# Kernel optimization log

Hardware: AMD Instinct MI355X
Metric: run time of the kernel (lower is better)

Reference implementation:

```python
import jax, jax.numpy as jnp
import numpy as np

D_MODEL = 1024
N_HEADS = 16
HEAD_DIM = D_MODEL // N_HEADS
B, T = 4, 2048
EPS = 1e-5


def _layernorm(x, w, b):
    mu = jnp.mean(x, axis=-1, keepdims=True)
    var = jnp.mean(jnp.square(x - mu), axis=-1, keepdims=True)
    return (x - mu) * jax.lax.rsqrt(var + EPS) * w + b


def _heads(x, w, b):
    # x: [B,T,D]; w stored [in,out] so y = x @ w + b (== torch Linear)
    y = x @ w + b
    return y.reshape(B, T, N_HEADS, HEAD_DIM).transpose(0, 2, 1, 3)  # [B,H,T,hd]


def _attention(q, k, v):
    scores = jnp.einsum('bhqd,bhkd->bhqk', q, k) / np.sqrt(HEAD_DIM).astype(np.float32)
    attn = jax.nn.softmax(scores, axis=-1)  # dropout is identity in eval mode
    o = jnp.einsum('bhqk,bhkd->bhqd', attn, v)
    return o.transpose(0, 2, 1, 3).reshape(B, T, D_MODEL)


def setup_inputs() -> dict:
    key = jax.random.key(0)
    ks = jax.random.split(key, 16)
    s = 1.0 / np.sqrt(D_MODEL)
    def lin(k, din, dout):
        kw, kb = jax.random.split(k)
        return (jax.random.uniform(kw, (din, dout), jnp.float32, -s, s),
                jax.random.uniform(kb, (dout,), jnp.float32, -s, s))
    inp = {}
    inp['temporal_tokens'] = jax.random.normal(ks[0], (B, T, D_MODEL), jnp.float32)
    inp['feature_tokens'] = jax.random.normal(ks[1], (B, T, D_MODEL), jnp.float32)
    names = ['qt', 'kf', 'vf', 'qf', 'kt', 'vt', 'ot', 'of']
    for i, n in enumerate(names):
        w, b = lin(ks[2 + i], D_MODEL, D_MODEL)
        inp[n + '_w'], inp[n + '_b'] = w, b
    inp['fus1_w'], inp['fus1_b'] = lin(ks[10], 2 * D_MODEL, D_MODEL)
    inp['fus2_w'], inp['fus2_b'] = lin(ks[11], D_MODEL, D_MODEL)
    for n in ['ln_fus', 'ln_t', 'ln_f']:
        inp[n + '_w'] = jnp.ones((D_MODEL,), jnp.float32)
        inp[n + '_b'] = jnp.zeros((D_MODEL,), jnp.float32)
    return inp


def reference(temporal_tokens, feature_tokens,
              qt_w, qt_b, kf_w, kf_b, vf_w, vf_b,
              qf_w, qf_b, kt_w, kt_b, vt_w, vt_b,
              ot_w, ot_b, of_w, of_b,
              fus1_w, fus1_b, fus2_w, fus2_b,
              ln_fus_w, ln_fus_b, ln_t_w, ln_t_b, ln_f_w, ln_f_b):
    # temporal -> feature cross attention
    Qt = _heads(temporal_tokens, qt_w, qt_b)
    Kf = _heads(feature_tokens, kf_w, kf_b)
    Vf = _heads(feature_tokens, vf_w, vf_b)
    attn_t = _attention(Qt, Kf, Vf) @ ot_w + ot_b
    fused_t = _layernorm(temporal_tokens + attn_t, ln_t_w, ln_t_b)
    # feature -> temporal cross attention
    Qf = _heads(feature_tokens, qf_w, qf_b)
    Kt = _heads(temporal_tokens, kt_w, kt_b)
    Vt = _heads(temporal_tokens, vt_w, vt_b)
    attn_f = _attention(Qf, Kt, Vt) @ of_w + of_b
    fused_f = _layernorm(feature_tokens + attn_f, ln_f_w, ln_f_b)
    # fusion MLP
    combined = jnp.concatenate([fused_t, fused_f], axis=-1)  # [B,T,2D]
    h = jax.nn.gelu(combined @ fus1_w + fus1_b, approximate=False)
    fused = _layernorm(h @ fus2_w + fus2_b, ln_fus_w, ln_fus_b)
    return fused
```

## Files before the change

### kernel.cpp

```cpp
#include <hip/hip_runtime.h>
#include <math.h>

typedef __attribute__((ext_vector_type(8))) short short8;
typedef __attribute__((ext_vector_type(4))) short short4v;
typedef __attribute__((ext_vector_type(4))) float floatx4;

#define GLOBAL_AS __attribute__((address_space(1)))
#define LDS_AS __attribute__((address_space(3)))

__device__ __forceinline__ float bf2f(unsigned short u) {
    unsigned int x = ((unsigned int)u) << 16;
    return __builtin_bit_cast(float, x);
}
__device__ __forceinline__ unsigned short f2bf(float f) {
    unsigned int u = __builtin_bit_cast(unsigned int, f);
    u += 0x7fffu + ((u >> 16) & 1u);
    return (unsigned short)(u >> 16);
}

__global__ __launch_bounds__(256) void cvt2_kernel(
    const float* __restrict__ a, const float* __restrict__ b,
    unsigned short* __restrict__ oa, unsigned short* __restrict__ ob)
{
    const int bx = blockIdx.x;
    const float* in = bx < 8192 ? a : b;
    unsigned short* out = bx < 8192 ? oa : ob;
    const size_t i = ((size_t)(bx & 8191) * 256 + threadIdx.x) * 4;
    float4 f = *(const float4*)(in + i);
    unsigned short o[4] = {f2bf(f.x), f2bf(f.y), f2bf(f.z), f2bf(f.w)};
    *(uint2*)(out + i) = *(const uint2*)o;
}

struct WX {
    const float* src[10];
    unsigned long long dst[10];
    int r64[10];
    int cum[11];
};

__global__ __launch_bounds__(256) void transpose_all_kernel(WX P, unsigned short* __restrict__ base)
{
    __shared__ unsigned short T[64][72];
    const int bx = blockIdx.x;
    int w = 0;
    #pragma unroll
    for (int i = 0; i < 10; ++i) if (bx >= P.cum[i + 1]) w = i + 1;
    const int tix = bx - P.cum[w];
    const int R = P.r64[w] * 64;
    const int r0 = (tix >> 4) * 64, c0 = (tix & 15) * 64;
    const float* in = P.src[w];
    unsigned short* out = base + P.dst[w];
    const int t = threadIdx.x;
    {
        const int r = t >> 2, cc = (t & 3) * 16;
        const float* p = in + (size_t)(r0 + r) * 1024 + c0 + cc;
        #pragma unroll
        for (int j = 0; j < 16; j += 4) {
            float4 f = *(const float4*)(p + j);
            T[cc + j + 0][r] = f2bf(f.x);
            T[cc + j + 1][r] = f2bf(f.y);
            T[cc + j + 2][r] = f2bf(f.z);
            T[cc + j + 3][r] = f2bf(f.w);
        }
    }
    __syncthreads();
    {
        const int c = t >> 2, rr = (t & 3) * 16;
        unsigned short* q = out + (size_t)(c0 + c) * R + r0 + rr;
        *(uint4*)(q)     = *(const uint4*)(&T[c][rr]);
        *(uint4*)(q + 8) = *(const uint4*)(&T[c][rr + 8]);
    }
}

#define GEMM_CORE(A_, B_, Kdim)                                               \
    const int tid = threadIdx.x;                                              \
    const int wave = tid >> 6, lane = tid & 63;                               \
    const int quad = lane >> 4, l16 = lane & 15;                              \
    const int wm = (wave & 1) * 64, wn = (wave >> 1) * 64;                    \
    const int srow8 = lane >> 3, c8 = lane & 7;                               \
    const int scol = (c8 ^ srow8) * 8;                                        \
    floatx4 acc[4][4];                                                        \
    _Pragma("unroll")                                                         \
    for (int i = 0; i < 4; ++i)                                               \
        _Pragma("unroll")                                                     \
        for (int j = 0; j < 4; ++j) acc[i][j] = (floatx4){0.f, 0.f, 0.f, 0.f};\
    const unsigned short* pa[4];                                              \
    const unsigned short* pb[4];                                              \
    _Pragma("unroll")                                                         \
    for (int i = 0; i < 4; ++i) {                                             \
        pa[i] = (A_) + (size_t)(bm + i * 32 + wave * 8 + srow8) * (Kdim) + scol; \
        pb[i] = (B_) + (size_t)(bn + i * 32 + wave * 8 + srow8) * (Kdim) + scol; \
    }                                                                         \
    int aoff[4][2], boff[4][2];                                               \
    _Pragma("unroll")                                                         \
    for (int i = 0; i < 4; ++i)                                               \
        _Pragma("unroll")                                                     \
        for (int s = 0; s < 2; ++s) {                                         \
            const int cg = ((s * 4 + quad) ^ (l16 & 7)) * 8;                  \
            aoff[i][s] = (wm + i * 16 + l16) * 64 + cg;                       \
            boff[i][s] = (wn + i * 16 + l16) * 64 + cg;                       \
        }                                                                     \
    for (int k0 = 0; k0 < (Kdim); k0 += 64) {                                 \
        _Pragma("unroll")                                                     \
        for (int i = 0; i < 4; ++i) {                                         \
            __builtin_amdgcn_global_load_lds((const GLOBAL_AS void*)(pa[i] + k0), \
                (LDS_AS void*)(As + i * 2048 + wave * 512), 16, 0, 0);        \
            __builtin_amdgcn_global_load_lds((const GLOBAL_AS void*)(pb[i] + k0), \
                (LDS_AS void*)(Bs + i * 2048 + wave * 512), 16, 0, 0);        \
        }                                                                     \
        __syncthreads();                                                      \
        _Pragma("unroll")                                                     \
        for (int s = 0; s < 2; ++s) {                                         \
            short8 af[4], bf[4];                                              \
            _Pragma("unroll")                                                 \
            for (int i = 0; i < 4; ++i) {                                     \
                af[i] = *(const short8*)&As[aoff[i][s]];                      \
                bf[i] = *(const short8*)&Bs[boff[i][s]];                      \
            }                                                                 \
            _Pragma("unroll")                                                 \
            for (int mi = 0; mi < 4; ++mi)                                    \
                _Pragma("unroll")                                             \
                for (int ni = 0; ni < 4; ++ni)                                \
                    acc[mi][ni] = __builtin_amdgcn_mfma_f32_16x16x32_bf16(    \
                        bf[ni], af[mi], acc[mi][ni], 0, 0, 0);                \
        }                                                                     \
        __syncthreads();                                                      \
    }

template <int MODE>
__global__ __launch_bounds__(256) void gemm_kernel(
    const unsigned short* __restrict__ A,
    const unsigned short* __restrict__ Wt,
    const float* __restrict__ bias,
    unsigned short* __restrict__ C,
    int N, int K)
{
    __shared__ unsigned short As[128 * 64];
    __shared__ unsigned short Bs[128 * 64];
    const int bm = blockIdx.x * 128, bn = blockIdx.y * 128;
    GEMM_CORE(A, Wt, K)

    float4 bv[4];
    #pragma unroll
    for (int ni = 0; ni < 4; ++ni)
        bv[ni] = *(const float4*)&bias[bn + wn + ni * 16 + quad * 4];
    #pragma unroll
    for (int mi = 0; mi < 4; ++mi) {
        const int m = bm + wm + mi * 16 + l16;
        #pragma unroll
        for (int ni = 0; ni < 4; ++ni) {
            const int n0 = bn + wn + ni * 16 + quad * 4;
            float v[4];
            #pragma unroll
            for (int r = 0; r < 4; ++r) v[r] = acc[mi][ni][r] + ((const float*)&bv[ni])[r];
            if (MODE == 2) {
                #pragma unroll
                for (int r = 0; r < 4; ++r)
                    v[r] = 0.5f * v[r] * (1.0f + erff(v[r] * 0.70710678118f));
            }
            unsigned short o[4] = {f2bf(v[0]), f2bf(v[1]), f2bf(v[2]), f2bf(v[3])};
            *(uint2*)&C[(size_t)m * N + n0] = *(const uint2*)o;
        }
    }
}

__global__ __launch_bounds__(256) void gemm_out_kernel(
    const unsigned short* __restrict__ A0, const unsigned short* __restrict__ W0,
    const float* __restrict__ bi0, const float* __restrict__ r0, unsigned short* __restrict__ C0,
    const unsigned short* __restrict__ A1, const unsigned short* __restrict__ W1,
    const float* __restrict__ bi1, const float* __restrict__ r1, unsigned short* __restrict__ C1)
{
    __shared__ unsigned short As[128 * 64];
    __shared__ unsigned short Bs[128 * 64];
    const int s1 = blockIdx.y >> 3;
    const unsigned short* A = s1 ? A1 : A0;
    const unsigned short* Wt = s1 ? W1 : W0;
    const float* bias = s1 ? bi1 : bi0;
    const float* resid = s1 ? r1 : r0;
    unsigned short* C = s1 ? C1 : C0;
    const int bm = blockIdx.x * 128, bn = (blockIdx.y & 7) * 128;
    GEMM_CORE(A, Wt, 1024)

    float4 bv[4];
    #pragma unroll
    for (int ni = 0; ni < 4; ++ni)
        bv[ni] = *(const float4*)&bias[bn + wn + ni * 16 + quad * 4];
    #pragma unroll
    for (int mi = 0; mi < 4; ++mi) {
        const int m = bm + wm + mi * 16 + l16;
        #pragma unroll
        for (int ni = 0; ni < 4; ++ni) {
            const int n0 = bn + wn + ni * 16 + quad * 4;
            float4 rv = *(const float4*)&resid[(size_t)m * 1024 + n0];
            float v[4];
            v[0] = acc[mi][ni][0] + ((const float*)&bv[ni])[0] + rv.x;
            v[1] = acc[mi][ni][1] + ((const float*)&bv[ni])[1] + rv.y;
            v[2] = acc[mi][ni][2] + ((const float*)&bv[ni])[2] + rv.z;
            v[3] = acc[mi][ni][3] + ((const float*)&bv[ni])[3] + rv.w;
            unsigned short o[4] = {f2bf(v[0]), f2bf(v[1]), f2bf(v[2]), f2bf(v[3])};
            *(uint2*)&C[(size_t)m * 1024 + n0] = *(const uint2*)o;
        }
    }
}

__global__ __launch_bounds__(256) void gemm_qkv_kernel(
    const unsigned short* __restrict__ At, const unsigned short* __restrict__ Wt3t,
    const float* __restrict__ tb0, const float* __restrict__ tb1, const float* __restrict__ tb2,
    unsigned short* __restrict__ to0, unsigned short* __restrict__ to1, unsigned short* __restrict__ to2,
    const unsigned short* __restrict__ Af, const unsigned short* __restrict__ Wt3f,
    const float* __restrict__ fb0, const float* __restrict__ fb1, const float* __restrict__ fb2,
    unsigned short* __restrict__ fo0, unsigned short* __restrict__ fo1, unsigned short* __restrict__ fo2,
    float scale0)
{
    __shared__ unsigned short As[128 * 64];
    __shared__ unsigned short Bs[128 * 64];
    const int str = blockIdx.y >= 24;
    const unsigned short* A = str ? Af : At;
    const unsigned short* Wt = str ? Wt3f : Wt3t;
    const int byy = str ? (blockIdx.y - 24) : blockIdx.y;
    const int buf = byy >> 3;
    const int bn = byy * 128;
    const int cn = (byy & 7) * 128;
    const float* bias = str ? (buf == 0 ? fb0 : (buf == 1 ? fb1 : fb2))
                            : (buf == 0 ? tb0 : (buf == 1 ? tb1 : tb2));
    unsigned short* C = str ? (buf == 0 ? fo0 : (buf == 1 ? fo1 : fo2))
                            : (buf == 0 ? to0 : (buf == 1 ? to1 : to2));
    const float scale = buf == 0 ? scale0 : 1.0f;
    const int bm = blockIdx.x * 128;
    GEMM_CORE(A, Wt, 1024)

    float4 bv[4];
    #pragma unroll
    for (int ni = 0; ni < 4; ++ni)
        bv[ni] = *(const float4*)&bias[cn + wn + ni * 16 + quad * 4];
    #pragma unroll
    for (int mi = 0; mi < 4; ++mi) {
        const int m = bm + wm + mi * 16 + l16;
        #pragma unroll
        for (int ni = 0; ni < 4; ++ni) {
            const int n0 = cn + wn + ni * 16 + quad * 4;
            unsigned short o[4];
            #pragma unroll
            for (int r = 0; r < 4; ++r)
                o[r] = f2bf((acc[mi][ni][r] + ((const float*)&bv[ni])[r]) * scale);
            if (buf == 2) {
                const int b = m >> 11, t = m & 2047;
                const int h = n0 >> 6, d0 = n0 & 63;
                const int tsw = t ^ ((d0 & 8) ? 4 : 0);
                unsigned short* vb = C + ((size_t)(b * 16 + h) * 64) * 2048 + tsw;
                #pragma unroll
                for (int r = 0; r < 4; ++r) vb[(size_t)(d0 + r) * 2048] = o[r];
            } else {
                *(uint2*)&C[(size_t)m * 1024 + n0] = *(const uint2*)o;
            }
        }
    }
}

__global__ __launch_bounds__(256) void flash_kernel(
    const unsigned short* __restrict__ Q0, const unsigned short* __restrict__ K0,
    const unsigned short* __restrict__ V0, unsigned short* __restrict__ O0,
    const unsigned short* __restrict__ Q1, const unsigned short* __restrict__ K1,
    const unsigned short* __restrict__ V1, unsigned short* __restrict__ O1)
{
    __shared__ unsigned short Ks[64 * 64];
    __shared__ unsigned short Vs[64 * 64];

    const int z = blockIdx.z;
    const int s1 = z >= 4;
    const unsigned short* Q = s1 ? Q1 : Q0;
    const unsigned short* Kmat = s1 ? K1 : K0;
    const unsigned short* Vtp = s1 ? V1 : V0;
    unsigned short* O = s1 ? O1 : O0;
    const int b = z & 3;
    const int q0 = blockIdx.x * 128;
    const int h = blockIdx.y;
    const int tid = threadIdx.x;
    const int wave = tid >> 6, lane = tid & 63;
    const int quad = lane >> 4, l16 = lane & 15;

    const unsigned short* qp = Q + (size_t)(b * 2048 + q0 + wave * 32 + l16) * 1024 + h * 64;
    short8 qf[2][2];
    qf[0][0] = *(const short8*)(qp + quad * 8);
    qf[0][1] = *(const short8*)(qp + 32 + quad * 8);
    qf[1][0] = *(const short8*)(qp + 16 * 1024 + quad * 8);
    qf[1][1] = *(const short8*)(qp + 16 * 1024 + 32 + quad * 8);

    const int srow8 = lane >> 3;
    const int c8 = lane & 7;
    const int rit0 = wave * 16 + srow8;
    const int rit1 = rit0 + 8;
    const int col0 = (c8 ^ (rit0 & 7)) * 8;
    const int col1 = (c8 ^ (rit1 & 7)) * 8;
    const unsigned short* kbase = Kmat + (size_t)b * 2048 * 1024 + h * 64;
    const unsigned short* vbase = Vtp + (size_t)(b * 16 + h) * 64 * 2048;
    unsigned short* lk0 = Ks + (wave * 16) * 64;
    unsigned short* lk1 = lk0 + 8 * 64;
    unsigned short* lv0 = Vs + (wave * 16) * 64;
    unsigned short* lv1 = lv0 + 8 * 64;

    int koff[4][2];
    #pragma unroll
    for (int nt = 0; nt < 4; ++nt)
        #pragma unroll
        for (int hh = 0; hh < 2; ++hh)
            koff[nt][hh] = (nt * 16 + l16) * 64 + (((hh * 4 + quad) ^ (l16 & 7)) * 8);
    int voff[4][4];
    #pragma unroll
    for (int dt = 0; dt < 4; ++dt)
        #pragma unroll
        for (int nt = 0; nt < 4; ++nt)
            voff[dt][nt] = (dt * 16 + l16) * 64 +
                           (((nt * 2 + (quad >> 1)) ^ (l16 & 7)) * 8) +
                           (((quad & 1) ^ (l16 >> 3)) * 4);

    floatx4 oa[2][4], la[2];
    #pragma unroll
    for (int qg = 0; qg < 2; ++qg) {
        la[qg] = (floatx4){0.f, 0.f, 0.f, 0.f};
        #pragma unroll
        for (int dt = 0; dt < 4; ++dt) oa[qg][dt] = (floatx4){0.f, 0.f, 0.f, 0.f};
    }
    const short4v vone = {(short)0x3F80, (short)0x3F80, (short)0x3F80, (short)0x3F80};

    for (int kt = 0; kt < 32; ++kt) {
        const unsigned short* kg0 = kbase + (size_t)(kt * 64 + rit0) * 1024 + col0;
        const unsigned short* kg1 = kbase + (size_t)(kt * 64 + rit1) * 1024 + col1;
        const unsigned short* vg0 = vbase + (size_t)rit0 * 2048 + kt * 64 + col0;
        const unsigned short* vg1 = vbase + (size_t)rit1 * 2048 + kt * 64 + col1;
        __builtin_amdgcn_global_load_lds((const GLOBAL_AS void*)kg0, (LDS_AS void*)lk0, 16, 0, 0);
        __builtin_amdgcn_global_load_lds((const GLOBAL_AS void*)kg1, (LDS_AS void*)lk1, 16, 0, 0);
        __builtin_amdgcn_global_load_lds((const GLOBAL_AS void*)vg0, (LDS_AS void*)lv0, 16, 0, 0);
        __builtin_amdgcn_global_load_lds((const GLOBAL_AS void*)vg1, (LDS_AS void*)lv1, 16, 0, 0);
        __syncthreads();

        short4v pf[2][4];
        #pragma unroll
        for (int nt = 0; nt < 4; ++nt) {
            short8 k0 = *(const short8*)&Ks[koff[nt][0]];
            short8 k1 = *(const short8*)&Ks[koff[nt][1]];
            #pragma unroll
            for (int qg = 0; qg < 2; ++qg) {
                floatx4 s = (floatx4){0.f, 0.f, 0.f, 0.f};
                s = __builtin_amdgcn_mfma_f32_16x16x32_bf16(k0, qf[qg][0], s, 0, 0, 0);
                s = __builtin_amdgcn_mfma_f32_16x16x32_bf16(k1, qf[qg][1], s, 0, 0, 0);
                float p0 = __builtin_amdgcn_exp2f(s[0]);
                float p1 = __builtin_amdgcn_exp2f(s[1]);
                float p2 = __builtin_amdgcn_exp2f(s[2]);
                float p3 = __builtin_amdgcn_exp2f(s[3]);
                unsigned u0 = __builtin_bit_cast(unsigned, p0) + 0x8000u;
                unsigned u1 = __builtin_bit_cast(unsigned, p1) + 0x8000u;
                unsigned u2 = __builtin_bit_cast(unsigned, p2) + 0x8000u;
                unsigned u3 = __builtin_bit_cast(unsigned, p3) + 0x8000u;
                union { unsigned u[2]; short4v s4; } pk;
                pk.u[0] = __builtin_amdgcn_perm(u1, u0, 0x07060302u);
                pk.u[1] = __builtin_amdgcn_perm(u3, u2, 0x07060302u);
                pf[qg][nt] = pk.s4;
                la[qg] = __builtin_amdgcn_mfma_f32_16x16x16bf16_1k(vone, pf[qg][nt], la[qg], 0, 0, 0);
            }
        }
        #pragma unroll
        for (int dt = 0; dt < 4; ++dt)
            #pragma unroll
            for (int nt = 0; nt < 4; ++nt) {
                short4v vf = *(const short4v*)&Vs[voff[dt][nt]];
                oa[0][dt] = __builtin_amdgcn_mfma_f32_16x16x16bf16_1k(vf, pf[0][nt], oa[0][dt], 0, 0, 0);
                oa[1][dt] = __builtin_amdgcn_mfma_f32_16x16x16bf16_1k(vf, pf[1][nt], oa[1][dt], 0, 0, 0);
            }
        __syncthreads();
    }

    #pragma unroll
    for (int qg = 0; qg < 2; ++qg) {
        const float linv = 1.0f / la[qg][0];
        unsigned short* orow = O + (size_t)(b * 2048 + q0 + wave * 32 + qg * 16 + l16) * 1024 + h * 64;
        #pragma unroll
        for (int dt = 0; dt < 4; ++dt) {
            unsigned short ob[4];
            #pragma unroll
            for (int r = 0; r < 4; ++r) ob[r] = f2bf(oa[qg][dt][r] * linv);
            *(uint2*)(orow + dt * 16 + quad * 4) = *(const uint2*)ob;
        }
    }
}

__global__ __launch_bounds__(256) void ln2_kernel(
    const unsigned short* __restrict__ in0, const unsigned short* __restrict__ in1,
    unsigned short* __restrict__ out,
    const float* __restrict__ w0, const float* __restrict__ b0,
    const float* __restrict__ w1, const float* __restrict__ b1)
{
    __shared__ float red[8];
    const int sel = blockIdx.x >> 13;
    const int row = blockIdx.x & 8191;
    const unsigned short* in = sel ? in1 : in0;
    const float* w = sel ? w1 : w0;
    const float* bb = sel ? b1 : b0;
    const int tid = threadIdx.x;
    const int wave = tid >> 6, lane = tid & 63;
    uint2 raw = *(const uint2*)(in + (size_t)row * 1024 + tid * 4);
    float v[4];
    v[0] = bf2f((unsigned short)(raw.x & 0xffffu));
    v[1] = bf2f((unsigned short)(raw.x >> 16));
    v[2] = bf2f((unsigned short)(raw.y & 0xffffu));
    v[3] = bf2f((unsigned short)(raw.y >> 16));
    float s = v[0] + v[1] + v[2] + v[3];
    float sq = v[0] * v[0] + v[1] * v[1] + v[2] * v[2] + v[3] * v[3];
    #pragma unroll
    for (int m = 1; m < 64; m <<= 1) { s += __shfl_xor(s, m); sq += __shfl_xor(sq, m); }
    if (lane == 0) { red[wave] = s; red[4 + wave] = sq; }
    __syncthreads();
    s = red[0] + red[1] + red[2] + red[3];
    sq = red[4] + red[5] + red[6] + red[7];
    const float mu = s * (1.0f / 1024.0f);
    const float var = sq * (1.0f / 1024.0f) - mu * mu;
    const float rstd = rsqrtf(var + 1e-5f);
    unsigned short ob[4];
    #pragma unroll
    for (int j = 0; j < 4; ++j)
        ob[j] = f2bf((v[j] - mu) * rstd * w[tid * 4 + j] + bb[tid * 4 + j]);
    *(uint2*)(out + (size_t)row * 2048 + sel * 1024 + tid * 4) = *(uint2*)ob;
}

__global__ __launch_bounds__(256) void ln_final_kernel(
    const unsigned short* __restrict__ in, float* __restrict__ out,
    const float* __restrict__ w, const float* __restrict__ bias)
{
    __shared__ float red[8];
    const int row = blockIdx.x;
    const int tid = threadIdx.x;
    const int wave = tid >> 6, lane = tid & 63;
    uint2 raw = *(const uint2*)(in + (size_t)row * 1024 + tid * 4);
    float v[4];
    v[0] = bf2f((unsigned short)(raw.x & 0xffffu));
    v[1] = bf2f((unsigned short)(raw.x >> 16));
    v[2] = bf2f((unsigned short)(raw.y & 0xffffu));
    v[3] = bf2f((unsigned short)(raw.y >> 16));
    float s = v[0] + v[1] + v[2] + v[3];
    float sq = v[0] * v[0] + v[1] * v[1] + v[2] * v[2] + v[3] * v[3];
    #pragma unroll
    for (int m = 1; m < 64; m <<= 1) { s += __shfl_xor(s, m); sq += __shfl_xor(sq, m); }
    if (lane == 0) { red[wave] = s; red[4 + wave] = sq; }
    __syncthreads();
    s = red[0] + red[1] + red[2] + red[3];
    sq = red[4] + red[5] + red[6] + red[7];
    const float mu = s * (1.0f / 1024.0f);
    const float var = sq * (1.0f / 1024.0f) - mu * mu;
    const float rstd = rsqrtf(var + 1e-5f);
    float o[4];
    #pragma unroll
    for (int j = 0; j < 4; ++j)
        o[j] = (v[j] - mu) * rstd * w[tid * 4 + j] + bias[tid * 4 + j];
    *(float4*)(out + (size_t)row * 1024 + tid * 4) = (float4){o[0], o[1], o[2], o[3]};
}

extern "C" void kernel_launch(void* const* d_in, const int* in_sizes, int n_in,
                              void* d_out, int out_size, void* d_ws, size_t ws_size,
                              hipStream_t stream)
{
    (void)in_sizes; (void)n_in; (void)out_size; (void)ws_size;
    const float* temporal = (const float*)d_in[0];
    const float* feature  = (const float*)d_in[1];
    const float* qt_w = (const float*)d_in[2];
    const float* qt_b = (const float*)d_in[3];
    const float* kf_w = (const float*)d_in[4];
    const float* kf_b = (const float*)d_in[5];
    const float* vf_w = (const float*)d_in[6];
    const float* vf_b = (const float*)d_in[7];
    const float* qf_w = (const float*)d_in[8];
    const float* qf_b = (const float*)d_in[9];
    const float* kt_w = (const float*)d_in[10];
    const float* kt_b = (const float*)d_in[11];
    const float* vt_w = (const float*)d_in[12];
    const float* vt_b = (const float*)d_in[13];
    const float* ot_w = (const float*)d_in[14];
    const float* ot_b = (const float*)d_in[15];
    const float* of_w = (const float*)d_in[16];
    const float* of_b = (const float*)d_in[17];
    const float* fus1_w = (const float*)d_in[18];
    const float* fus1_b = (const float*)d_in[19];
    const float* fus2_w = (const float*)d_in[20];
    const float* fus2_b = (const float*)d_in[21];
    const float* ln_fus_w = (const float*)d_in[22];
    const float* ln_fus_b = (const float*)d_in[23];
    const float* ln_t_w = (const float*)d_in[24];
    const float* ln_t_b = (const float*)d_in[25];
    const float* ln_f_w = (const float*)d_in[26];
    const float* ln_f_b = (const float*)d_in[27];

    unsigned short* p = (unsigned short*)d_ws;
    const size_t EW = 1024ull * 1024;
    const size_t ET = 8192ull * 1024;
    unsigned short* WT3t = p;
    unsigned short* WT3f = p + 3 * EW;
    unsigned short* WTot = p + 6 * EW;
    unsigned short* WTof = p + 7 * EW;
    unsigned short* WTf1 = p + 8 * EW;
    unsigned short* WTf2 = p + 10 * EW;
    size_t off = 11 * EW;
    unsigned short* Tb = p + off; off += ET;
    unsigned short* Fb = p + off; off += ET;
    unsigned short* Qt = p + off; off += ET;
    unsigned short* Kt = p + off; off += ET;
    unsigned short* Vt = p + off; off += ET;
    unsigned short* Qf = p + off; off += ET;
    unsigned short* Kf = p + off; off += ET;
    unsigned short* Vf = p + off; off += ET;
    unsigned short* VfT = p + off; off += ET;
    unsigned short* VtT = p + off; off += ET;
    unsigned short* attnT = p + off; off += ET;
    unsigned short* attnF = p + off; off += ET;
    unsigned short* yT = Qt;
    unsigned short* yF = Qf;
    unsigned short* comb = Kt;
    unsigned short* hbuf = Kf;
    unsigned short* y2 = Vf;
    (void)Vt;

    const float SC = 0.125f * 1.4426950408889634f;

    cvt2_kernel<<<16384, 256, 0, stream>>>(temporal, feature, Tb, Fb);

    {
        WX P;
        const float* srcs[10] = {qt_w, kt_w, vt_w, qf_w, kf_w, vf_w,
                                 ot_w, of_w, fus1_w, fus2_w};
        unsigned long long dsts[10] = {
            0, EW, 2 * EW,
            3 * EW, 4 * EW, 5 * EW,
            6 * EW, 7 * EW, 8 * EW, 10 * EW};
        int cum = 0;
        P.cum[0] = 0;
        for (int i = 0; i < 10; ++i) {
            P.src[i] = srcs[i];
            P.dst[i] = dsts[i];
            P.r64[i] = (i == 8) ? 32 : 16;
            cum += P.r64[i] * 16;
            P.cum[i + 1] = cum;
        }
        transpose_all_kernel<<<cum, 256, 0, stream>>>(P, p);
    }

    const dim3 gb(256);
    gemm_qkv_kernel<<<dim3(64, 48), gb, 0, stream>>>(
        Tb, WT3t, qt_b, kt_b, vt_b, Qt, Kt, VtT,
        Fb, WT3f, qf_b, kf_b, vf_b, Qf, Kf, VfT, SC);
    flash_kernel<<<dim3(16, 16, 8), gb, 0, stream>>>(
        Qt, Kf, VfT, attnT, Qf, Kt, VtT, attnF);
    gemm_out_kernel<<<dim3(64, 16), gb, 0, stream>>>(
        attnT, WTot, ot_b, temporal, yT,
        attnF, WTof, of_b, feature,  yF);
    ln2_kernel<<<16384, gb, 0, stream>>>(yT, yF, comb, ln_t_w, ln_t_b, ln_f_w, ln_f_b);
    gemm_kernel<2><<<dim3(64, 8), gb, 0, stream>>>(comb, WTf1, fus1_b, hbuf, 1024, 2048);
    gemm_kernel<0><<<dim3(64, 8), gb, 0, stream>>>(hbuf, WTf2, fus2_b, y2, 1024, 1024);
    ln_final_kernel<<<8192, gb, 0, stream>>>(y2, (float*)d_out, ln_fus_w, ln_fus_b);
}
```

Baseline: 673.8 us.

## Use 32x32 MFMA in GEMMs, fuse input conversion, remap flash grid

Switches the shared GEMM core from 16x16x32 to 32x32x16 bf16 MFMA with 2x2 accumulator tiles, and rewrites every epilogue for the new output layout. This cuts LDS fragment loads per MFMA and the instruction count. The activation fp32-to-bf16 conversion is merged into the weight transpose kernel, removing one launch. The flash attention grid is flattened to 1D with a remap so consecutive blocks spread across XCDs while sharing the same head, aiming for better L2 locality.

```diff
diff --git a/kernel.cpp b/kernel.cpp
--- a/kernel.cpp
+++ b/kernel.cpp
@@ -4,6 +4,7 @@
 typedef __attribute__((ext_vector_type(8))) short short8;
 typedef __attribute__((ext_vector_type(4))) short short4v;
 typedef __attribute__((ext_vector_type(4))) float floatx4;
+typedef __attribute__((ext_vector_type(16))) float floatx16;
 
 #define GLOBAL_AS __attribute__((address_space(1)))
 #define LDS_AS __attribute__((address_space(3)))
@@ -16,19 +17,6 @@
     unsigned int u = __builtin_bit_cast(unsigned int, f);
     u += 0x7fffu + ((u >> 16) & 1u);
     return (unsigned short)(u >> 16);
-}
-
-__global__ __launch_bounds__(256) void cvt2_kernel(
-    const float* __restrict__ a, const float* __restrict__ b,
-    unsigned short* __restrict__ oa, unsigned short* __restrict__ ob)
-{
-    const int bx = blockIdx.x;
-    const float* in = bx < 8192 ? a : b;
-    unsigned short* out = bx < 8192 ? oa : ob;
-    const size_t i = ((size_t)(bx & 8191) * 256 + threadIdx.x) * 4;
-    float4 f = *(const float4*)(in + i);
-    unsigned short o[4] = {f2bf(f.x), f2bf(f.y), f2bf(f.z), f2bf(f.w)};
-    *(uint2*)(out + i) = *(const uint2*)o;
 }
 
 struct WX {
@@ -38,10 +26,27 @@
     int cum[11];
 };
 
-__global__ __launch_bounds__(256) void transpose_all_kernel(WX P, unsigned short* __restrict__ base)
+__global__ __launch_bounds__(256) void prep_kernel(
+    WX P, unsigned short* __restrict__ base,
+    const float* __restrict__ ta, const float* __restrict__ tb,
+    unsigned short* __restrict__ oa, unsigned short* __restrict__ ob)
 {
     __shared__ unsigned short T[64][72];
     const int bx = blockIdx.x;
+    if (bx >= P.cum[10]) {
+        const int cb = bx - P.cum[10];
+        const float* in = cb < 1024 ? ta : tb;
+        unsigned short* out = cb < 1024 ? oa : ob;
+        const size_t b0 = (size_t)(cb & 1023) * 8192;
+        #pragma unroll
+        for (int j = 0; j < 8; ++j) {
+            const size_t i = b0 + (size_t)j * 1024 + threadIdx.x * 4;
+            float4 f = *(const float4*)(in + i);
+            unsigned short o[4] = {f2bf(f.x), f2bf(f.y), f2bf(f.z), f2bf(f.w)};
+            *(uint2*)(out + i) = *(const uint2*)o;
+        }
+        return;
+    }
     int w = 0;
     #pragma unroll
     for (int i = 0; i < 10; ++i) if (bx >= P.cum[i + 1]) w = i + 1;
@@ -75,15 +80,17 @@
 #define GEMM_CORE(A_, B_, Kdim)                                               \
     const int tid = threadIdx.x;                                              \
     const int wave = tid >> 6, lane = tid & 63;                               \
-    const int quad = lane >> 4, l16 = lane & 15;                              \
+    const int l32 = lane & 31, hi = lane >> 5;                                \
     const int wm = (wave & 1) * 64, wn = (wave >> 1) * 64;                    \
     const int srow8 = lane >> 3, c8 = lane & 7;                               \
     const int scol = (c8 ^ srow8) * 8;                                        \
-    floatx4 acc[4][4];                                                        \
+    floatx16 acc[2][2];                                                       \
     _Pragma("unroll")                                                         \
-    for (int i = 0; i < 4; ++i)                                               \
+    for (int i = 0; i < 2; ++i)                                               \
         _Pragma("unroll")                                                     \
-        for (int j = 0; j < 4; ++j) acc[i][j] = (floatx4){0.f, 0.f, 0.f, 0.f};\
+        for (int j = 0; j < 2; ++j)                                           \
+            _Pragma("unroll")                                                 \
+            for (int r = 0; r < 16; ++r) acc[i][j][r] = 0.f;                  \
     const unsigned short* pa[4];                                              \
     const unsigned short* pb[4];                                              \
     _Pragma("unroll")                                                         \
@@ -91,14 +98,14 @@
         pa[i] = (A_) + (size_t)(bm + i * 32 + wave * 8 + srow8) * (Kdim) + scol; \
         pb[i] = (B_) + (size_t)(bn + i * 32 + wave * 8 + srow8) * (Kdim) + scol; \
     }                                                                         \
-    int aoff[4][2], boff[4][2];                                               \
+    int aoff[2][4], boff[2][4];                                               \
     _Pragma("unroll")                                                         \
-    for (int i = 0; i < 4; ++i)                                               \
+    for (int f = 0; f < 2; ++f)                                               \
         _Pragma("unroll")                                                     \
-        for (int s = 0; s < 2; ++s) {                                         \
-            const int cg = ((s * 4 + quad) ^ (l16 & 7)) * 8;                  \
-            aoff[i][s] = (wm + i * 16 + l16) * 64 + cg;                       \
-            boff[i][s] = (wn + i * 16 + l16) * 64 + cg;                       \
+        for (int s = 0; s < 4; ++s) {                                         \
+            const int cg = ((s * 2 + hi) ^ (l32 & 7)) * 8;                    \
+            aoff[f][s] = (wm + f * 32 + l32) * 64 + cg;                       \
+            boff[f][s] = (wn + f * 32 + l32) * 64 + cg;                       \
         }                                                                     \
     for (int k0 = 0; k0 < (Kdim); k0 += 64) {                                 \
         _Pragma("unroll")                                                     \
@@ -110,18 +117,18 @@
         }                                                                     \
         __syncthreads();                                                      \
         _Pragma("unroll")                                                     \
-        for (int s = 0; s < 2; ++s) {                                         \
-            short8 af[4], bf[4];                                              \
+        for (int s = 0; s < 4; ++s) {                                         \
+            short8 af[2], bf[2];                                              \
             _Pragma("unroll")                                                 \
-            for (int i = 0; i < 4; ++i) {                                     \
-                af[i] = *(const short8*)&As[aoff[i][s]];                      \
-                bf[i] = *(const short8*)&Bs[boff[i][s]];                      \
+            for (int f = 0; f < 2; ++f) {                                     \
+                af[f] = *(const short8*)&As[aoff[f][s]];                      \
+                bf[f] = *(const short8*)&Bs[boff[f][s]];                      \
             }                                                                 \
             _Pragma("unroll")                                                 \
-            for (int mi = 0; mi < 4; ++mi)                                    \
+            for (int mi = 0; mi < 2; ++mi)                                    \
                 _Pragma("unroll")                                             \
-                for (int ni = 0; ni < 4; ++ni)                                \
-                    acc[mi][ni] = __builtin_amdgcn_mfma_f32_16x16x32_bf16(    \
+                for (int ni = 0; ni < 2; ++ni)                                \
+                    acc[mi][ni] = __builtin_amdgcn_mfma_f32_32x32x16_bf16(    \
                         bf[ni], af[mi], acc[mi][ni], 0, 0, 0);                \
         }                                                                     \
         __syncthreads();                                                      \
@@ -140,26 +147,27 @@
     const int bm = blockIdx.x * 128, bn = blockIdx.y * 128;
     GEMM_CORE(A, Wt, K)
 
-    float4 bv[4];
-    #pragma unroll
-    for (int ni = 0; ni < 4; ++ni)
-        bv[ni] = *(const float4*)&bias[bn + wn + ni * 16 + quad * 4];
-    #pragma unroll
-    for (int mi = 0; mi < 4; ++mi) {
-        const int m = bm + wm + mi * 16 + l16;
-        #pragma unroll
-        for (int ni = 0; ni < 4; ++ni) {
-            const int n0 = bn + wn + ni * 16 + quad * 4;
-            float v[4];
+    #pragma unroll
+    for (int mi = 0; mi < 2; ++mi) {
+        const int m = bm + wm + mi * 32 + l32;
+        #pragma unroll
+        for (int ni = 0; ni < 2; ++ni) {
             #pragma unroll
-            for (int r = 0; r < 4; ++r) v[r] = acc[mi][ni][r] + ((const float*)&bv[ni])[r];
-            if (MODE == 2) {
+            for (int rg = 0; rg < 4; ++rg) {
+                const int n0 = bn + wn + ni * 32 + rg * 8 + hi * 4;
+                float4 bv = *(const float4*)&bias[n0];
+                float v[4];
                 #pragma unroll
                 for (int r = 0; r < 4; ++r)
-                    v[r] = 0.5f * v[r] * (1.0f + erff(v[r] * 0.70710678118f));
+                    v[r] = acc[mi][ni][rg * 4 + r] + ((const float*)&bv)[r];
+                if (MODE == 2) {
+                    #pragma unroll
+                    for (int r = 0; r < 4; ++r)
+                        v[r] = 0.5f * v[r] * (1.0f + erff(v[r] * 0.70710678118f));
+                }
+                unsigned short o[4] = {f2bf(v[0]), f2bf(v[1]), f2bf(v[2]), f2bf(v[3])};
+                *(uint2*)&C[(size_t)m * N + n0] = *(const uint2*)o;
             }
-            unsigned short o[4] = {f2bf(v[0]), f2bf(v[1]), f2bf(v[2]), f2bf(v[3])};
-            *(uint2*)&C[(size_t)m * N + n0] = *(const uint2*)o;
         }
     }
 }
@@ -181,24 +189,24 @@
     const int bm = blockIdx.x * 128, bn = (blockIdx.y & 7) * 128;
     GEMM_CORE(A, Wt, 1024)
 
-    float4 bv[4];
-    #pragma unroll
-    for (int ni = 0; ni < 4; ++ni)
-        bv[ni] = *(const float4*)&bias[bn + wn + ni * 16 + quad * 4];
-    #pragma unroll
-    for (int mi = 0; mi < 4; ++mi) {
-        const int m = bm + wm + mi * 16 + l16;
-        #pragma unroll
-        for (int ni = 0; ni < 4; ++ni) {
-            const int n0 = bn + wn + ni * 16 + quad * 4;
-            float4 rv = *(const float4*)&resid[(size_t)m * 1024 + n0];
-            float v[4];
-            v[0] = acc[mi][ni][0] + ((const float*)&bv[ni])[0] + rv.x;
-            v[1] = acc[mi][ni][1] + ((const float*)&bv[ni])[1] + rv.y;
-            v[2] = acc[mi][ni][2] + ((const float*)&bv[ni])[2] + rv.z;
-            v[3] = acc[mi][ni][3] + ((const float*)&bv[ni])[3] + rv.w;
-            unsigned short o[4] = {f2bf(v[0]), f2bf(v[1]), f2bf(v[2]), f2bf(v[3])};
-            *(uint2*)&C[(size_t)m * 1024 + n0] = *(const uint2*)o;
+    #pragma unroll
+    for (int mi = 0; mi < 2; ++mi) {
+        const int m = bm + wm + mi * 32 + l32;
+        #pragma unroll
+        for (int ni = 0; ni < 2; ++ni) {
+            #pragma unroll
+            for (int rg = 0; rg < 4; ++rg) {
+                const int n0 = bn + wn + ni * 32 + rg * 8 + hi * 4;
+                float4 bv = *(const float4*)&bias[n0];
+                float4 rv = *(const float4*)&resid[(size_t)m * 1024 + n0];
+                float v[4];
+                v[0] = acc[mi][ni][rg * 4 + 0] + bv.x + rv.x;
+                v[1] = acc[mi][ni][rg * 4 + 1] + bv.y + rv.y;
+                v[2] = acc[mi][ni][rg * 4 + 2] + bv.z + rv.z;
+                v[3] = acc[mi][ni][rg * 4 + 3] + bv.w + rv.w;
+                unsigned short o[4] = {f2bf(v[0]), f2bf(v[1]), f2bf(v[2]), f2bf(v[3])};
+                *(uint2*)&C[(size_t)m * 1024 + n0] = *(const uint2*)o;
+            }
         }
     }
 }
@@ -229,29 +237,29 @@
     const int bm = blockIdx.x * 128;
     GEMM_CORE(A, Wt, 1024)
 
-    float4 bv[4];
-    #pragma unroll
-    for (int ni = 0; ni < 4; ++ni)
-        bv[ni] = *(const float4*)&bias[cn + wn + ni * 16 + quad * 4];
-    #pragma unroll
-    for (int mi = 0; mi < 4; ++mi) {
-        const int m = bm + wm + mi * 16 + l16;
-        #pragma unroll
-        for (int ni = 0; ni < 4; ++ni) {
-            const int n0 = cn + wn + ni * 16 + quad * 4;
-            unsigned short o[4];
+    #pragma unroll
+    for (int mi = 0; mi < 2; ++mi) {
+        const int m = bm + wm + mi * 32 + l32;
+        #pragma unroll
+        for (int ni = 0; ni < 2; ++ni) {
             #pragma unroll
-            for (int r = 0; r < 4; ++r)
-                o[r] = f2bf((acc[mi][ni][r] + ((const float*)&bv[ni])[r]) * scale);
-            if (buf == 2) {
-                const int b = m >> 11, t = m & 2047;
-                const int h = n0 >> 6, d0 = n0 & 63;
-                const int tsw = t ^ ((d0 & 8) ? 4 : 0);
-                unsigned short* vb = C + ((size_t)(b * 16 + h) * 64) * 2048 + tsw;
+            for (int rg = 0; rg < 4; ++rg) {
+                const int n0 = cn + wn + ni * 32 + rg * 8 + hi * 4;
+                float4 bv = *(const float4*)&bias[n0];
+                unsigned short o[4];
                 #pragma unroll
-                for (int r = 0; r < 4; ++r) vb[(size_t)(d0 + r) * 2048] = o[r];
-            } else {
-                *(uint2*)&C[(size_t)m * 1024 + n0] = *(const uint2*)o;
+                for (int r = 0; r < 4; ++r)
+                    o[r] = f2bf((acc[mi][ni][rg * 4 + r] + ((const float*)&bv)[r]) * scale);
+                if (buf == 2) {
+                    const int b = m >> 11, t = m & 2047;
+                    const int h = n0 >> 6, d0 = n0 & 63;
+                    const int tsw = t ^ ((d0 & 8) ? 4 : 0);
+                    unsigned short* vb = C + ((size_t)(b * 16 + h) * 64) * 2048 + tsw;
+                    #pragma unroll
+                    for (int r = 0; r < 4; ++r) vb[(size_t)(d0 + r) * 2048] = o[r];
+                } else {
+                    *(uint2*)&C[(size_t)m * 1024 + n0] = *(const uint2*)o;
+                }
             }
         }
     }
@@ -266,15 +274,18 @@
     __shared__ unsigned short Ks[64 * 64];
     __shared__ unsigned short Vs[64 * 64];
 
-    const int z = blockIdx.z;
-    const int s1 = z >= 4;
+    const int bid = blockIdx.x;
+    const int p = (bid & 7) * 16 + (bid >> 7);
+    const int qt = (bid >> 3) & 15;
+    const int s1 = p >= 64;
+    const int rem = p & 63;
+    const int b = rem >> 4, h = rem & 15;
     const unsigned short* Q = s1 ? Q1 : Q0;
     const unsigned short* Kmat = s1 ? K1 : K0;
     const unsigned short* Vtp = s1 ? V1 : V0;
     unsigned short* O = s1 ? O1 : O0;
-    const int b = z & 3;
-    const int q0 = blockIdx.x * 128;
-    const int h = blockIdx.y;
+    const int q0 = qt * 128;
+
     const int tid = threadIdx.x;
     const int wave = tid >> 6, lane = tid & 63;
     const int quad = lane >> 4, l16 = lane & 15;
@@ -519,8 +530,6 @@
 
     const float SC = 0.125f * 1.4426950408889634f;
 
-    cvt2_kernel<<<16384, 256, 0, stream>>>(temporal, feature, Tb, Fb);
-
     {
         WX P;
         const float* srcs[10] = {qt_w, kt_w, vt_w, qf_w, kf_w, vf_w,
@@ -538,14 +547,14 @@
             cum += P.r64[i] * 16;
             P.cum[i + 1] = cum;
         }
-        transpose_all_kernel<<<cum, 256, 0, stream>>>(P, p);
+        prep_kernel<<<cum + 2048, 256, 0, stream>>>(P, p, temporal, feature, Tb, Fb);
     }
 
     const dim3 gb(256);
     gemm_qkv_kernel<<<dim3(64, 48), gb, 0, stream>>>(
         Tb, WT3t, qt_b, kt_b, vt_b, Qt, Kt, VtT,
         Fb, WT3f, qf_b, kf_b, vf_b, Qf, Kf, VfT, SC);
-    flash_kernel<<<dim3(16, 16, 8), gb, 0, stream>>>(
+    flash_kernel<<<2048, gb, 0, stream>>>(
         Qt, Kf, VfT, attnT, Qf, Kt, VtT, attnF);
     gemm_out_kernel<<<dim3(64, 16), gb, 0, stream>>>(
         attnT, WTot, ot_b, temporal, yT,
```

New measurement: 662.7 us. No clear change (-1.6%).
